# Kernel tuning notes

Measured on AMD Instinct MI355X. Metric: run time of the kernel, lower is better.

Reference implementation:

```python
import jax, jax.numpy as jnp
import numpy as np

N_NODES = 50000
N_EDGES = 1600000
IN_DIM = 256
HID = 128
HEADS = 1
N_CLASSES = 40
NEG_SLOPE = 0.2


def gat_conv(x, W, a_src, a_dst, b, src, dst, concat):
    """PyG GATConv (eval mode). x: [N, F_in]; W: [H*C, F_in]; a_*: [H, C]; b: bias."""
    N = x.shape[0]
    H, C = a_src.shape
    h = (x @ W.T).reshape(N, H, C)                       # [N, H, C]
    alpha_src = jnp.sum(h * a_src, axis=-1)              # [N, H]
    alpha_dst = jnp.sum(h * a_dst, axis=-1)              # [N, H]
    e = jax.nn.leaky_relu(alpha_src[src] + alpha_dst[dst], NEG_SLOPE)  # [E, H]
    # scatter-softmax over incoming edges of each destination node
    m = jax.ops.segment_max(e, dst, num_segments=N)
    m = jnp.where(jnp.isfinite(m), m, 0.0)               # nodes with no in-edges
    ex = jnp.exp(e - m[dst])
    denom = jax.ops.segment_sum(ex, dst, num_segments=N)
    alpha = ex / jnp.maximum(denom[dst], 1e-16)          # [E, H]
    out = jax.ops.segment_sum(h[src] * alpha[..., None], dst, num_segments=N)  # [N, H, C]
    out = out.reshape(N, H * C) if concat else out.mean(axis=1)
    return out + b


def setup_inputs() -> dict:
    key = jax.random.key(0)
    ks = jax.random.split(key, 10)
    glorot = lambda k, shape: jax.random.normal(k, shape, jnp.float32) * np.sqrt(2.0 / (shape[0] + shape[-1]))
    x = jax.random.normal(ks[0], (N_NODES, IN_DIM), jnp.float32)
    edge_index = jax.random.randint(ks[1], (2, N_EDGES), 0, N_NODES, jnp.int64)
    # layer 0: in=IN_DIM -> hidden, heads=HEADS, concat=True
    W0 = glorot(ks[2], (HEADS * HID, IN_DIM))
    a_src0 = glorot(ks[3], (HEADS, HID))
    a_dst0 = glorot(ks[4], (HEADS, HID))
    b0 = jnp.zeros((HEADS * HID,), jnp.float32)
    # layer 1: in=hidden*heads -> n_classes, concat=False
    W1 = glorot(ks[5], (HEADS * N_CLASSES, HEADS * HID))
    a_src1 = glorot(ks[6], (HEADS, N_CLASSES))
    a_dst1 = glorot(ks[7], (HEADS, N_CLASSES))
    b1 = jnp.zeros((N_CLASSES,), jnp.float32)
    return {"x": x, "edge_index": edge_index,
            "W0": W0, "a_src0": a_src0, "a_dst0": a_dst0, "b0": b0,
            "W1": W1, "a_src1": a_src1, "a_dst1": a_dst1, "b1": b1}


def reference(x, edge_index, W0, a_src0, a_dst0, b0, W1, a_src1, a_dst1, b1):
    N = x.shape[0]
    # PyG GATConv default add_self_loops=True (each layer adds them transiently)
    loop = jnp.arange(N, dtype=edge_index.dtype)
    src = jnp.concatenate([edge_index[0], loop])
    dst = jnp.concatenate([edge_index[1], loop])
    h = gat_conv(x, W0, a_src0, a_dst0, b0, src, dst, concat=True)
    h = jax.nn.relu(h)  # dropout is identity in eval mode
    out = gat_conv(h, W1, a_src1, a_dst1, b1, src, dst, concat=False)
    return out
```

## Files before the change

### kernel.cpp

```cpp
#include <hip/hip_runtime.h>
#include <hip/hip_bf16.h>

#define N_NODES 50000
#define N_EDGES 1600000
#define ET (N_EDGES + N_NODES)
#define IN_DIM 256
#define HID 128
#define NCLS 40
#define NEG 0.2f
#define NBUCK 391
#define CHUNK 4096
#define CAP 5120
#define SCATB ((ET + CHUNK - 1) / CHUNK)
#define GEMMB ((N_NODES + 63) / 64)

typedef short bf16x8 __attribute__((ext_vector_type(8)));
typedef float f32x4  __attribute__((ext_vector_type(4)));

__device__ __forceinline__ unsigned pk2(float a, float b) {
    __hip_bfloat16 ha = __float2bfloat16(a), hb = __float2bfloat16(b);
    unsigned short ua = *(unsigned short*)&ha, ub = *(unsigned short*)&hb;
    return (unsigned)ua | ((unsigned)ub << 16);
}
__device__ __forceinline__ float blo(unsigned u) { return __uint_as_float(u << 16); }
__device__ __forceinline__ float bhi(unsigned u) { return __uint_as_float(u & 0xffff0000u); }

__global__ void k_init(int* __restrict__ cursor) {
    int i = blockIdx.x * 256 + threadIdx.x;
    if (i < NBUCK) cursor[i] = i * CAP;
}

__global__ __launch_bounds__(256) void k_fused(
    const int* __restrict__ ei, int* __restrict__ cursor, unsigned int* __restrict__ buf,
    const float* __restrict__ x, const float* __restrict__ W0,
    const float* __restrict__ a_s, const float* __restrict__ a_d,
    unsigned short* __restrict__ h0b, float* __restrict__ as0, float* __restrict__ ad0) {
    __shared__ unsigned pool[6912];
    int t = threadIdx.x;

    if (blockIdx.x < SCATB) {
        int* sd    = (int*)pool;
        int* hist  = (int*)pool + 4096;
        int* wbase = (int*)pool + 4487;
        for (int i = t; i < NBUCK; i += 256) hist[i] = 0;
        __syncthreads();
        int base = blockIdx.x * CHUNK;
        #pragma unroll
        for (int j = 0; j < 16; ++j) {
            int i = base + j * 256 + t;
            int d = -1;
            if (i < ET) d = (i < N_EDGES) ? ei[N_EDGES + i] : (i - N_EDGES);
            sd[j * 256 + t] = d;
            if (d >= 0) atomicAdd(&hist[d >> 7], 1);
        }
        __syncthreads();
        for (int i = t; i < NBUCK; i += 256) {
            int h = hist[i];
            wbase[i] = h ? atomicAdd(&cursor[i], h) : 0;
            hist[i] = 0;
        }
        __syncthreads();
        #pragma unroll
        for (int j = 0; j < 16; ++j) {
            int i = base + j * 256 + t;
            int d = sd[j * 256 + t];
            if (d >= 0) {
                int s_ = (i < N_EDGES) ? ei[i] : d;
                int b = d >> 7;
                int off = atomicAdd(&hist[b], 1);
                buf[wbase[b] + off] = ((unsigned)(d & 127) << 16) | (unsigned)s_;
            }
        }
        return;
    }

    unsigned* sA = pool;
    unsigned* sB = pool + 2304;
    int n0 = (blockIdx.x - SCATB) * 64;
    int w = t >> 6, lane = t & 63;
    int rw = lane & 15, q = lane >> 4;
    f32x4 acc[8];
    #pragma unroll
    for (int n = 0; n < 8; ++n) acc[n] = (f32x4){0.f, 0.f, 0.f, 0.f};

    for (int kc = 0; kc < IN_DIM; kc += 64) {
        #pragma unroll
        for (int i = 0; i < 4; ++i) {
            int f = i * 256 + t;
            int r = f >> 4, fq = f & 15;
            float4 v = make_float4(0.f, 0.f, 0.f, 0.f);
            if (n0 + r < N_NODES)
                v = *(const float4*)&x[(size_t)(n0 + r) * IN_DIM + kc + fq * 4];
            *(uint2*)&sA[r * 36 + fq * 2] = make_uint2(pk2(v.x, v.y), pk2(v.z, v.w));
        }
        #pragma unroll
        for (int i = 0; i < 8; ++i) {
            int f = i * 256 + t;
            int c = f >> 4, fq = f & 15;
            float4 v = *(const float4*)&W0[(size_t)c * IN_DIM + kc + fq * 4];
            *(uint2*)&sB[c * 36 + fq * 2] = make_uint2(pk2(v.x, v.y), pk2(v.z, v.w));
        }
        __syncthreads();
        #pragma unroll
        for (int ks = 0; ks < 2; ++ks) {
            bf16x8 af = *(const bf16x8*)((const unsigned short*)sA + (16 * w + rw) * 72 + ks * 32 + q * 8);
            #pragma unroll
            for (int n = 0; n < 8; ++n) {
                bf16x8 bfr = *(const bf16x8*)((const unsigned short*)sB + (n * 16 + rw) * 72 + ks * 32 + q * 8);
                acc[n] = __builtin_amdgcn_mfma_f32_16x16x32_bf16(af, bfr, acc[n], 0, 0, 0);
            }
        }
        __syncthreads();
    }

    float asv[8], adv[8];
    #pragma unroll
    for (int n = 0; n < 8; ++n) { asv[n] = a_s[n * 16 + rw]; adv[n] = a_d[n * 16 + rw]; }
    float ps[4] = {0.f, 0.f, 0.f, 0.f}, pd[4] = {0.f, 0.f, 0.f, 0.f};
    #pragma unroll
    for (int n = 0; n < 8; ++n)
        #pragma unroll
        for (int reg = 0; reg < 4; ++reg) {
            float vv = acc[n][reg];
            ps[reg] += vv * asv[n];
            pd[reg] += vv * adv[n];
        }
    #pragma unroll
    for (int reg = 0; reg < 4; ++reg) {
        int node = n0 + 16 * w + q * 4 + reg;
        if (node < N_NODES) {
            #pragma unroll
            for (int n = 0; n < 8; ++n) {
                __hip_bfloat16 hb = __float2bfloat16(acc[n][reg]);
                h0b[(size_t)node * HID + n * 16 + rw] = *(unsigned short*)&hb;
            }
        }
    }
    #pragma unroll
    for (int reg = 0; reg < 4; ++reg)
        #pragma unroll
        for (int off = 1; off < 16; off <<= 1) {
            ps[reg] += __shfl_xor(ps[reg], off);
            pd[reg] += __shfl_xor(pd[reg], off);
        }
    if (rw == 0) {
        #pragma unroll
        for (int reg = 0; reg < 4; ++reg) {
            int node = n0 + 16 * w + q * 4 + reg;
            if (node < N_NODES) { as0[node] = ps[reg]; ad0[node] = pd[reg]; }
        }
    }
}

__global__ __launch_bounds__(256) void k_bucket_build(const unsigned int* __restrict__ buf,
                                                      const int* __restrict__ cursor,
                                                      int* __restrict__ rp, int* __restrict__ re,
                                                      int* __restrict__ csr) {
    __shared__ int cnt[128], rpl[128], cur[128];
    int b = blockIdx.x;
    int t = threadIdx.x;
    int lo = b * CAP, hi = cursor[b];
    if (t < 128) cnt[t] = 0;
    __syncthreads();
    for (int i = lo + t; i < hi; i += 256) atomicAdd(&cnt[buf[i] >> 16], 1);
    __syncthreads();
    if (t == 0) {
        int run = 0;
        #pragma unroll
        for (int l = 0; l < 128; ++l) { rpl[l] = run; run += cnt[l]; }
    }
    __syncthreads();
    if (t < 128) {
        int node = b * 128 + t;
        if (node < N_NODES) { rp[node] = lo + rpl[t]; re[node] = lo + rpl[t] + cnt[t]; }
        cur[t] = 0;
    }
    __syncthreads();
    for (int i = lo + t; i < hi; i += 256) {
        unsigned v = buf[i];
        int dl = v >> 16;
        int off = atomicAdd(&cur[dl], 1);
        csr[lo + rpl[dl] + off] = (int)(v & 0xffffu);
    }
}

__global__ __launch_bounds__(256) void k_agg0(
    const uint4* __restrict__ h0q, const float* __restrict__ as, const float* __restrict__ ad,
    const int* __restrict__ rp, const int* __restrict__ re, const int* __restrict__ csr,
    const float* __restrict__ bias, unsigned short* __restrict__ actb) {
    __shared__ float sw_[4][64];
    __shared__ int   ss_[4][64];
    int wid = threadIdx.x >> 6, lane = threadIdx.x & 63;
    int q = lane >> 4, ql = lane & 15;
    int node = blockIdx.x * 4 + wid;
    int start = rp[node], end = re[node];
    float ad_n = ad[node];
    float a0 = 0.f, a1 = 0.f, a2 = 0.f, a3 = 0.f;
    float a4 = 0.f, a5 = 0.f, a6 = 0.f, a7 = 0.f, den = 0.f;
    for (int base = start; base < end; base += 64) {
        int mm = end - base; if (mm > 64) mm = 64;
        int s_l = 0; float w_l = 0.f;
        if (lane < mm) {
            s_l = csr[base + lane];
            float e = as[s_l] + ad_n;
            e = (e > 0.f) ? e : NEG * e;
            w_l = __expf(e);
            den += w_l;
        }
        ss_[wid][lane] = s_l;
        sw_[wid][lane] = w_l;
        for (int jj = 0; jj < mm; jj += 16) {
            int i0 = jj + q, i1 = i0 + 4, i2 = i0 + 8, i3 = i0 + 12;
            int   s0 = ss_[wid][i0], s1 = ss_[wid][i1], s2 = ss_[wid][i2], s3 = ss_[wid][i3];
            float w0 = sw_[wid][i0], w1 = sw_[wid][i1], w2 = sw_[wid][i2], w3 = sw_[wid][i3];
            uint4 u0 = h0q[(size_t)s0 * 16 + ql];
            uint4 u1 = h0q[(size_t)s1 * 16 + ql];
            uint4 u2 = h0q[(size_t)s2 * 16 + ql];
            uint4 u3 = h0q[(size_t)s3 * 16 + ql];
            a0 += w0 * blo(u0.x) + w1 * blo(u1.x) + w2 * blo(u2.x) + w3 * blo(u3.x);
            a1 += w0 * bhi(u0.x) + w1 * bhi(u1.x) + w2 * bhi(u2.x) + w3 * bhi(u3.x);
            a2 += w0 * blo(u0.y) + w1 * blo(u1.y) + w2 * blo(u2.y) + w3 * blo(u3.y);
            a3 += w0 * bhi(u0.y) + w1 * bhi(u1.y) + w2 * bhi(u2.y) + w3 * bhi(u3.y);
            a4 += w0 * blo(u0.z) + w1 * blo(u1.z) + w2 * blo(u2.z) + w3 * blo(u3.z);
            a5 += w0 * bhi(u0.z) + w1 * bhi(u1.z) + w2 * bhi(u2.z) + w3 * bhi(u3.z);
            a6 += w0 * blo(u0.w) + w1 * blo(u1.w) + w2 * blo(u2.w) + w3 * blo(u3.w);
            a7 += w0 * bhi(u0.w) + w1 * bhi(u1.w) + w2 * bhi(u2.w) + w3 * bhi(u3.w);
        }
    }
    #pragma unroll
    for (int off = 32; off; off >>= 1) den += __shfl_xor(den, off);
    a0 += __shfl_xor(a0, 16); a0 += __shfl_xor(a0, 32);
    a1 += __shfl_xor(a1, 16); a1 += __shfl_xor(a1, 32);
    a2 += __shfl_xor(a2, 16); a2 += __shfl_xor(a2, 32);
    a3 += __shfl_xor(a3, 16); a3 += __shfl_xor(a3, 32);
    a4 += __shfl_xor(a4, 16); a4 += __shfl_xor(a4, 32);
    a5 += __shfl_xor(a5, 16); a5 += __shfl_xor(a5, 32);
    a6 += __shfl_xor(a6, 16); a6 += __shfl_xor(a6, 32);
    a7 += __shfl_xor(a7, 16); a7 += __shfl_xor(a7, 32);
    if (lane < 16) {
        float inv = 1.f / fmaxf(den, 1e-16f);
        float4 b0v = *(const float4*)&bias[ql * 8];
        float4 b1v = *(const float4*)&bias[ql * 8 + 4];
        float r0 = fmaxf(a0 * inv + b0v.x, 0.f);
        float r1 = fmaxf(a1 * inv + b0v.y, 0.f);
        float r2 = fmaxf(a2 * inv + b0v.z, 0.f);
        float r3 = fmaxf(a3 * inv + b0v.w, 0.f);
        float r4 = fmaxf(a4 * inv + b1v.x, 0.f);
        float r5 = fmaxf(a5 * inv + b1v.y, 0.f);
        float r6 = fmaxf(a6 * inv + b1v.z, 0.f);
        float r7 = fmaxf(a7 * inv + b1v.w, 0.f);
        *(uint4*)&actb[(size_t)node * HID + ql * 8] =
            make_uint4(pk2(r0, r1), pk2(r2, r3), pk2(r4, r5), pk2(r6, r7));
    }
}

__global__ __launch_bounds__(128) void k_gemm1(
    const unsigned short* __restrict__ actb, const float* __restrict__ W1,
    const float* __restrict__ a_s, const float* __restrict__ a_d,
    unsigned short* __restrict__ h1b, float* __restrict__ as1, float* __restrict__ ad1) {
    __shared__ float w1l[NCLS * HID];
    __shared__ float av[NCLS], adv[NCLS];
    int t = threadIdx.x;
    #pragma unroll
    for (int i = 0; i < 10; ++i) {
        int j = t + 128 * i;
        ((float4*)w1l)[j] = ((const float4*)W1)[j];
    }
    if (t < NCLS) { av[t] = a_s[t]; adv[t] = a_d[t]; }
    __syncthreads();
    int n = blockIdx.x * 128 + t;
    if (n >= N_NODES) return;
    const uint4* ar = (const uint4*)(actb + (size_t)n * HID);
    float acc[NCLS];
    #pragma unroll
    for (int c = 0; c < NCLS; ++c) acc[c] = 0.f;
    for (int k0 = 0; k0 < HID; k0 += 8) {
        uint4 v = ar[k0 >> 3];
        float x0 = blo(v.x), x1 = bhi(v.x), x2 = blo(v.y), x3 = bhi(v.y);
        float x4 = blo(v.z), x5 = bhi(v.z), x6 = blo(v.w), x7 = bhi(v.w);
        #pragma unroll
        for (int c = 0; c < NCLS; ++c) {
            const float* wr = &w1l[c * HID + k0];
            acc[c] += x0 * wr[0] + x1 * wr[1] + x2 * wr[2] + x3 * wr[3]
                    + x4 * wr[4] + x5 * wr[5] + x6 * wr[6] + x7 * wr[7];
        }
    }
    float ps = 0.f, pd = 0.f;
    #pragma unroll
    for (int c = 0; c < NCLS; ++c) { ps += acc[c] * av[c]; pd += acc[c] * adv[c]; }
    unsigned pk_[20];
    #pragma unroll
    for (int c = 0; c < 20; ++c) pk_[c] = pk2(acc[2 * c], acc[2 * c + 1]);
    #pragma unroll
    for (int i = 0; i < 5; ++i)
        *(uint4*)&h1b[(size_t)n * NCLS + i * 8] = make_uint4(pk_[4*i], pk_[4*i+1], pk_[4*i+2], pk_[4*i+3]);
    as1[n] = ps; ad1[n] = pd;
}

__global__ __launch_bounds__(256) void k_agg1(
    const uint2* __restrict__ h1u, const float* __restrict__ as, const float* __restrict__ ad,
    const int* __restrict__ rp, const int* __restrict__ re, const int* __restrict__ csr,
    const float* __restrict__ bias, float* __restrict__ out) {
    __shared__ float sw_[4][64];
    __shared__ int   ss_[4][64];
    int wid = threadIdx.x >> 6, lane = threadIdx.x & 63;
    int q = lane >> 4, ql = lane & 15;
    int off10 = (ql < 10) ? ql : 0;
    int node = blockIdx.x * 4 + wid;
    int start = rp[node], end = re[node];
    float ad_n = ad[node];
    float a0 = 0.f, a1 = 0.f, a2 = 0.f, a3 = 0.f, den = 0.f;
    for (int base = start; base < end; base += 64) {
        int mm = end - base; if (mm > 64) mm = 64;
        int s_l = 0; float w_l = 0.f;
        if (lane < mm) {
            s_l = csr[base + lane];
            float e = as[s_l] + ad_n;
            e = (e > 0.f) ? e : NEG * e;
            w_l = __expf(e);
            den += w_l;
        }
        ss_[wid][lane] = s_l;
        sw_[wid][lane] = w_l;
        for (int jj = 0; jj < mm; jj += 16) {
            int i0 = jj + q, i1 = i0 + 4, i2 = i0 + 8, i3 = i0 + 12;
            int   s0 = ss_[wid][i0], s1 = ss_[wid][i1], s2 = ss_[wid][i2], s3 = ss_[wid][i3];
            float w0 = sw_[wid][i0], w1 = sw_[wid][i1], w2 = sw_[wid][i2], w3 = sw_[wid][i3];
            uint2 u0 = h1u[(size_t)s0 * 10 + off10];
            uint2 u1 = h1u[(size_t)s1 * 10 + off10];
            uint2 u2 = h1u[(size_t)s2 * 10 + off10];
            uint2 u3 = h1u[(size_t)s3 * 10 + off10];
            a0 += w0 * blo(u0.x) + w1 * blo(u1.x) + w2 * blo(u2.x) + w3 * blo(u3.x);
            a1 += w0 * bhi(u0.x) + w1 * bhi(u1.x) + w2 * bhi(u2.x) + w3 * bhi(u3.x);
            a2 += w0 * blo(u0.y) + w1 * blo(u1.y) + w2 * blo(u2.y) + w3 * blo(u3.y);
            a3 += w0 * bhi(u0.y) + w1 * bhi(u1.y) + w2 * bhi(u2.y) + w3 * bhi(u3.y);
        }
    }
    #pragma unroll
    for (int off = 32; off; off >>= 1) den += __shfl_xor(den, off);
    a0 += __shfl_xor(a0, 16); a0 += __shfl_xor(a0, 32);
    a1 += __shfl_xor(a1, 16); a1 += __shfl_xor(a1, 32);
    a2 += __shfl_xor(a2, 16); a2 += __shfl_xor(a2, 32);
    a3 += __shfl_xor(a3, 16); a3 += __shfl_xor(a3, 32);
    if (lane < 10) {
        float inv = 1.f / fmaxf(den, 1e-16f);
        float4 b4 = *(const float4*)&bias[ql * 4];
        float4 r;
        r.x = a0 * inv + b4.x;
        r.y = a1 * inv + b4.y;
        r.z = a2 * inv + b4.z;
        r.w = a3 * inv + b4.w;
        *(float4*)&out[(size_t)node * NCLS + ql * 4] = r;
    }
}

extern "C" void kernel_launch(void* const* d_in, const int* in_sizes, int n_in,
                              void* d_out, int out_size, void* d_ws, size_t ws_size,
                              hipStream_t stream) {
    const float* x    = (const float*)d_in[0];
    const int*   ei   = (const int*)d_in[1];
    const float* W0   = (const float*)d_in[2];
    const float* a_s0 = (const float*)d_in[3];
    const float* a_d0 = (const float*)d_in[4];
    const float* b0   = (const float*)d_in[5];
    const float* W1   = (const float*)d_in[6];
    const float* a_s1 = (const float*)d_in[7];
    const float* a_d1 = (const float*)d_in[8];
    const float* b1   = (const float*)d_in[9];

    char* p = (char*)d_ws;
    auto alloc = [&](size_t bytes) { void* q = p; p += (bytes + 255) & ~size_t(255); return q; };
    unsigned short* h0b  = (unsigned short*)alloc((size_t)N_NODES * HID * 2);
    unsigned int*   buf  = (unsigned int*)alloc((size_t)NBUCK * CAP * 4);
    int*   csr    = (int*)alloc((size_t)NBUCK * CAP * 4);
    unsigned short* h1b  = (unsigned short*)alloc(((size_t)N_NODES * NCLS + 32) * 2);
    unsigned short* actb = (unsigned short*)alloc((size_t)N_NODES * HID * 2);
    float* as0    = (float*)alloc((size_t)N_NODES * 4);
    float* ad0    = (float*)alloc((size_t)N_NODES * 4);
    float* as1    = (float*)alloc((size_t)N_NODES * 4);
    float* ad1    = (float*)alloc((size_t)N_NODES * 4);
    int*   rp     = (int*)alloc((size_t)N_NODES * 4);
    int*   re     = (int*)alloc((size_t)N_NODES * 4);
    int*   cursor = (int*)alloc((size_t)NBUCK * 4);

    k_init<<<(NBUCK + 255) / 256, 256, 0, stream>>>(cursor);
    k_fused<<<SCATB + GEMMB, 256, 0, stream>>>(ei, cursor, buf, x, W0, a_s0, a_d0, h0b, as0, ad0);
    k_bucket_build<<<NBUCK, 256, 0, stream>>>(buf, cursor, rp, re, csr);
    k_agg0<<<N_NODES / 4, 256, 0, stream>>>((const uint4*)h0b, as0, ad0, rp, re, csr, b0, actb);
    k_gemm1<<<(N_NODES + 127) / 128, 128, 0, stream>>>(actb, W1, a_s1, a_d1, h1b, as1, ad1);
    k_agg1<<<N_NODES / 4, 256, 0, stream>>>((const uint2*)h1b, as1, ad1, rp, re, csr, b1, (float*)d_out);
}
```

Before: 271.3 us.

## Merge all stages into one persistent cooperative kernel with grid syncs

Replaces the six separate kernel launches with a single cooperative persistent kernel. The scatter/GEMM, CSR bucket build, layer-0 aggregation, layer-1 GEMM and layer-1 aggregation each run as a grid-stride phase, separated by grid.sync(). The grid is sized from the occupancy query, with launch bounds set to 4 blocks per CU. This is meant to remove launch overhead and inter-kernel gaps. In exchange it adds grid-wide barriers, lower per-phase occupancy, and register pressure from holding every phase in one kernel.

```diff
diff --git a/kernel.cpp b/kernel.cpp
--- a/kernel.cpp
+++ b/kernel.cpp
@@ -1,5 +1,8 @@
 #include <hip/hip_runtime.h>
 #include <hip/hip_bf16.h>
+#include <hip/hip_cooperative_groups.h>
+
+namespace cg = cooperative_groups;
 
 #define N_NODES 50000
 #define N_EDGES 1600000
@@ -25,332 +28,341 @@
 __device__ __forceinline__ float blo(unsigned u) { return __uint_as_float(u << 16); }
 __device__ __forceinline__ float bhi(unsigned u) { return __uint_as_float(u & 0xffff0000u); }
 
-__global__ void k_init(int* __restrict__ cursor) {
-    int i = blockIdx.x * 256 + threadIdx.x;
-    if (i < NBUCK) cursor[i] = i * CAP;
-}
-
-__global__ __launch_bounds__(256) void k_fused(
+__global__ __launch_bounds__(256, 4) void k_mega(
     const int* __restrict__ ei, int* __restrict__ cursor, unsigned int* __restrict__ buf,
     const float* __restrict__ x, const float* __restrict__ W0,
-    const float* __restrict__ a_s, const float* __restrict__ a_d,
-    unsigned short* __restrict__ h0b, float* __restrict__ as0, float* __restrict__ ad0) {
+    const float* __restrict__ a_s0, const float* __restrict__ a_d0,
+    unsigned short* __restrict__ h0b, float* __restrict__ as0, float* __restrict__ ad0,
+    int* __restrict__ rp, int* __restrict__ re, int* __restrict__ csr,
+    const float* __restrict__ b0, unsigned short* __restrict__ actb,
+    const float* __restrict__ W1, const float* __restrict__ a_s1, const float* __restrict__ a_d1,
+    unsigned short* __restrict__ h1b, float* __restrict__ as1, float* __restrict__ ad1,
+    const float* __restrict__ b1, float* __restrict__ out) {
     __shared__ unsigned pool[6912];
-    int t = threadIdx.x;
-
-    if (blockIdx.x < SCATB) {
-        int* sd    = (int*)pool;
-        int* hist  = (int*)pool + 4096;
-        int* wbase = (int*)pool + 4487;
-        for (int i = t; i < NBUCK; i += 256) hist[i] = 0;
-        __syncthreads();
-        int base = blockIdx.x * CHUNK;
+    cg::grid_group grid = cg::this_grid();
+    const int t = threadIdx.x;
+    const int nb = gridDim.x;
+
+    for (int task = blockIdx.x; task < SCATB + GEMMB; task += nb) {
+        if (task < SCATB) {
+            int* sd    = (int*)pool;
+            int* hist  = (int*)pool + 4096;
+            int* wbase = (int*)pool + 4487;
+            for (int i = t; i < NBUCK; i += 256) hist[i] = 0;
+            __syncthreads();
+            int base = task * CHUNK;
+            #pragma unroll
+            for (int j = 0; j < 16; ++j) {
+                int i = base + j * 256 + t;
+                int d = -1;
+                if (i < ET) d = (i < N_EDGES) ? ei[N_EDGES + i] : (i - N_EDGES);
+                sd[j * 256 + t] = d;
+                if (d >= 0) atomicAdd(&hist[d >> 7], 1);
+            }
+            __syncthreads();
+            for (int i = t; i < NBUCK; i += 256) {
+                int h = hist[i];
+                wbase[i] = i * CAP + (h ? atomicAdd(&cursor[i], h) : 0);
+                hist[i] = 0;
+            }
+            __syncthreads();
+            #pragma unroll
+            for (int j = 0; j < 16; ++j) {
+                int i = base + j * 256 + t;
+                int d = sd[j * 256 + t];
+                if (d >= 0) {
+                    int s_ = (i < N_EDGES) ? ei[i] : d;
+                    int bb = d >> 7;
+                    int off = atomicAdd(&hist[bb], 1);
+                    buf[wbase[bb] + off] = ((unsigned)(d & 127) << 16) | (unsigned)s_;
+                }
+            }
+        } else {
+            unsigned* sA = pool;
+            unsigned* sB = pool + 2304;
+            int n0 = (task - SCATB) * 64;
+            int w = t >> 6, lane = t & 63;
+            int rw = lane & 15, q = lane >> 4;
+            f32x4 acc[8];
+            #pragma unroll
+            for (int n = 0; n < 8; ++n) acc[n] = (f32x4){0.f, 0.f, 0.f, 0.f};
+            for (int kc = 0; kc < IN_DIM; kc += 64) {
+                #pragma unroll
+                for (int i = 0; i < 4; ++i) {
+                    int f = i * 256 + t;
+                    int r = f >> 4, fq = f & 15;
+                    float4 v = make_float4(0.f, 0.f, 0.f, 0.f);
+                    if (n0 + r < N_NODES)
+                        v = *(const float4*)&x[(size_t)(n0 + r) * IN_DIM + kc + fq * 4];
+                    *(uint2*)&sA[r * 36 + fq * 2] = make_uint2(pk2(v.x, v.y), pk2(v.z, v.w));
+                }
+                #pragma unroll
+                for (int i = 0; i < 8; ++i) {
+                    int f = i * 256 + t;
+                    int c = f >> 4, fq = f & 15;
+                    float4 v = *(const float4*)&W0[(size_t)c * IN_DIM + kc + fq * 4];
+                    *(uint2*)&sB[c * 36 + fq * 2] = make_uint2(pk2(v.x, v.y), pk2(v.z, v.w));
+                }
+                __syncthreads();
+                #pragma unroll
+                for (int ks = 0; ks < 2; ++ks) {
+                    bf16x8 af = *(const bf16x8*)((const unsigned short*)sA + (16 * w + rw) * 72 + ks * 32 + q * 8);
+                    #pragma unroll
+                    for (int n = 0; n < 8; ++n) {
+                        bf16x8 bfr = *(const bf16x8*)((const unsigned short*)sB + (n * 16 + rw) * 72 + ks * 32 + q * 8);
+                        acc[n] = __builtin_amdgcn_mfma_f32_16x16x32_bf16(af, bfr, acc[n], 0, 0, 0);
+                    }
+                }
+                __syncthreads();
+            }
+            float asv[8], adv[8];
+            #pragma unroll
+            for (int n = 0; n < 8; ++n) { asv[n] = a_s0[n * 16 + rw]; adv[n] = a_d0[n * 16 + rw]; }
+            float ps[4] = {0.f, 0.f, 0.f, 0.f}, pd[4] = {0.f, 0.f, 0.f, 0.f};
+            #pragma unroll
+            for (int n = 0; n < 8; ++n)
+                #pragma unroll
+                for (int reg = 0; reg < 4; ++reg) {
+                    float vv = acc[n][reg];
+                    ps[reg] += vv * asv[n];
+                    pd[reg] += vv * adv[n];
+                }
+            #pragma unroll
+            for (int reg = 0; reg < 4; ++reg) {
+                int node = n0 + 16 * w + q * 4 + reg;
+                if (node < N_NODES) {
+                    #pragma unroll
+                    for (int n = 0; n < 8; ++n) {
+                        __hip_bfloat16 hb = __float2bfloat16(acc[n][reg]);
+                        h0b[(size_t)node * HID + n * 16 + rw] = *(unsigned short*)&hb;
+                    }
+                }
+            }
+            #pragma unroll
+            for (int reg = 0; reg < 4; ++reg)
+                #pragma unroll
+                for (int off = 1; off < 16; off <<= 1) {
+                    ps[reg] += __shfl_xor(ps[reg], off);
+                    pd[reg] += __shfl_xor(pd[reg], off);
+                }
+            if (rw == 0) {
+                #pragma unroll
+                for (int reg = 0; reg < 4; ++reg) {
+                    int node = n0 + 16 * w + q * 4 + reg;
+                    if (node < N_NODES) { as0[node] = ps[reg]; ad0[node] = pd[reg]; }
+                }
+            }
+        }
+        __syncthreads();
+    }
+    grid.sync();
+
+    for (int b = blockIdx.x; b < NBUCK; b += nb) {
+        int* cnt = (int*)pool;
+        int* rpl = (int*)pool + 128;
+        int* cur = (int*)pool + 256;
+        int lo = b * CAP, hi = lo + cursor[b];
+        if (t < 128) cnt[t] = 0;
+        __syncthreads();
+        for (int i = lo + t; i < hi; i += 256) atomicAdd(&cnt[buf[i] >> 16], 1);
+        __syncthreads();
+        if (t == 0) {
+            int run = 0;
+            #pragma unroll
+            for (int l = 0; l < 128; ++l) { rpl[l] = run; run += cnt[l]; }
+        }
+        __syncthreads();
+        if (t < 128) {
+            int node = b * 128 + t;
+            if (node < N_NODES) { rp[node] = lo + rpl[t]; re[node] = lo + rpl[t] + cnt[t]; }
+            cur[t] = 0;
+        }
+        __syncthreads();
+        for (int i = lo + t; i < hi; i += 256) {
+            unsigned v = buf[i];
+            int dl = v >> 16;
+            int off = atomicAdd(&cur[dl], 1);
+            csr[lo + rpl[dl] + off] = (int)(v & 0xffffu);
+        }
+        __syncthreads();
+    }
+    grid.sync();
+
+    {
+        float* swp = (float*)pool;
+        int*   ssp = (int*)pool + 256;
+        const uint4* h0q = (const uint4*)h0b;
+        int wid = t >> 6, lane = t & 63;
+        int q = lane >> 4, ql = lane & 15;
+        for (int g = blockIdx.x; g < N_NODES / 4; g += nb) {
+            int node = g * 4 + wid;
+            int start = rp[node], end = re[node];
+            float ad_n = ad0[node];
+            float a0 = 0.f, a1 = 0.f, a2 = 0.f, a3 = 0.f;
+            float a4 = 0.f, a5 = 0.f, a6 = 0.f, a7 = 0.f, den = 0.f;
+            for (int base = start; base < end; base += 64) {
+                int mm = end - base; if (mm > 64) mm = 64;
+                int s_l = 0; float w_l = 0.f;
+                if (lane < mm) {
+                    s_l = csr[base + lane];
+                    float e = as0[s_l] + ad_n;
+                    e = (e > 0.f) ? e : NEG * e;
+                    w_l = __expf(e);
+                    den += w_l;
+                }
+                ssp[wid * 64 + lane] = s_l;
+                swp[wid * 64 + lane] = w_l;
+                for (int jj = 0; jj < mm; jj += 16) {
+                    int i0 = jj + q, i1 = i0 + 4, i2 = i0 + 8, i3 = i0 + 12;
+                    int   s0 = ssp[wid * 64 + i0], s1 = ssp[wid * 64 + i1];
+                    int   s2 = ssp[wid * 64 + i2], s3 = ssp[wid * 64 + i3];
+                    float w0 = swp[wid * 64 + i0], w1 = swp[wid * 64 + i1];
+                    float w2 = swp[wid * 64 + i2], w3 = swp[wid * 64 + i3];
+                    uint4 u0 = h0q[(size_t)s0 * 16 + ql];
+                    uint4 u1 = h0q[(size_t)s1 * 16 + ql];
+                    uint4 u2 = h0q[(size_t)s2 * 16 + ql];
+                    uint4 u3 = h0q[(size_t)s3 * 16 + ql];
+                    a0 += w0 * blo(u0.x) + w1 * blo(u1.x) + w2 * blo(u2.x) + w3 * blo(u3.x);
+                    a1 += w0 * bhi(u0.x) + w1 * bhi(u1.x) + w2 * bhi(u2.x) + w3 * bhi(u3.x);
+                    a2 += w0 * blo(u0.y) + w1 * blo(u1.y) + w2 * blo(u2.y) + w3 * blo(u3.y);
+                    a3 += w0 * bhi(u0.y) + w1 * bhi(u1.y) + w2 * bhi(u2.y) + w3 * bhi(u3.y);
+                    a4 += w0 * blo(u0.z) + w1 * blo(u1.z) + w2 * blo(u2.z) + w3 * blo(u3.z);
+                    a5 += w0 * bhi(u0.z) + w1 * bhi(u1.z) + w2 * bhi(u2.z) + w3 * bhi(u3.z);
+                    a6 += w0 * blo(u0.w) + w1 * blo(u1.w) + w2 * blo(u2.w) + w3 * blo(u3.w);
+                    a7 += w0 * bhi(u0.w) + w1 * bhi(u1.w) + w2 * bhi(u2.w) + w3 * bhi(u3.w);
+                }
+            }
+            #pragma unroll
+            for (int off = 32; off; off >>= 1) den += __shfl_xor(den, off);
+            a0 += __shfl_xor(a0, 16); a0 += __shfl_xor(a0, 32);
+            a1 += __shfl_xor(a1, 16); a1 += __shfl_xor(a1, 32);
+            a2 += __shfl_xor(a2, 16); a2 += __shfl_xor(a2, 32);
+            a3 += __shfl_xor(a3, 16); a3 += __shfl_xor(a3, 32);
+            a4 += __shfl_xor(a4, 16); a4 += __shfl_xor(a4, 32);
+            a5 += __shfl_xor(a5, 16); a5 += __shfl_xor(a5, 32);
+            a6 += __shfl_xor(a6, 16); a6 += __shfl_xor(a6, 32);
+            a7 += __shfl_xor(a7, 16); a7 += __shfl_xor(a7, 32);
+            if (lane < 16) {
+                float inv = 1.f / fmaxf(den, 1e-16f);
+                float4 b0v = *(const float4*)&b0[ql * 8];
+                float4 b1v = *(const float4*)&b0[ql * 8 + 4];
+                float r0 = fmaxf(a0 * inv + b0v.x, 0.f);
+                float r1 = fmaxf(a1 * inv + b0v.y, 0.f);
+                float r2 = fmaxf(a2 * inv + b0v.z, 0.f);
+                float r3 = fmaxf(a3 * inv + b0v.w, 0.f);
+                float r4 = fmaxf(a4 * inv + b1v.x, 0.f);
+                float r5 = fmaxf(a5 * inv + b1v.y, 0.f);
+                float r6 = fmaxf(a6 * inv + b1v.z, 0.f);
+                float r7 = fmaxf(a7 * inv + b1v.w, 0.f);
+                *(uint4*)&actb[(size_t)node * HID + ql * 8] =
+                    make_uint4(pk2(r0, r1), pk2(r2, r3), pk2(r4, r5), pk2(r6, r7));
+            }
+        }
+    }
+    grid.sync();
+
+    {
+        float* w1l = (float*)pool;
+        float* av  = (float*)pool + 5120;
+        float* adv = (float*)pool + 5160;
         #pragma unroll
-        for (int j = 0; j < 16; ++j) {
-            int i = base + j * 256 + t;
-            int d = -1;
-            if (i < ET) d = (i < N_EDGES) ? ei[N_EDGES + i] : (i - N_EDGES);
-            sd[j * 256 + t] = d;
-            if (d >= 0) atomicAdd(&hist[d >> 7], 1);
-        }
-        __syncthreads();
-        for (int i = t; i < NBUCK; i += 256) {
-            int h = hist[i];
-            wbase[i] = h ? atomicAdd(&cursor[i], h) : 0;
-            hist[i] = 0;
-        }
-        __syncthreads();
-        #pragma unroll
-        for (int j = 0; j < 16; ++j) {
-            int i = base + j * 256 + t;
-            int d = sd[j * 256 + t];
-            if (d >= 0) {
-                int s_ = (i < N_EDGES) ? ei[i] : d;
-                int b = d >> 7;
-                int off = atomicAdd(&hist[b], 1);
-                buf[wbase[b] + off] = ((unsigned)(d & 127) << 16) | (unsigned)s_;
-            }
-        }
-        return;
+        for (int i = 0; i < 5; ++i) {
+            int j = t + 256 * i;
+            ((float4*)w1l)[j] = ((const float4*)W1)[j];
+        }
+        if (t < NCLS) { av[t] = a_s1[t]; adv[t] = a_d1[t]; }
+        __syncthreads();
+        for (int g = blockIdx.x; g < (N_NODES + 255) / 256; g += nb) {
+            int n = g * 256 + t;
+            if (n < N_NODES) {
+                const uint4* ar = (const uint4*)(actb + (size_t)n * HID);
+                float acc[NCLS];
+                #pragma unroll
+                for (int c = 0; c < NCLS; ++c) acc[c] = 0.f;
+                for (int k0 = 0; k0 < HID; k0 += 8) {
+                    uint4 v = ar[k0 >> 3];
+                    float x0 = blo(v.x), x1 = bhi(v.x), x2 = blo(v.y), x3 = bhi(v.y);
+                    float x4 = blo(v.z), x5 = bhi(v.z), x6 = blo(v.w), x7 = bhi(v.w);
+                    #pragma unroll
+                    for (int c = 0; c < NCLS; ++c) {
+                        const float* wr = &w1l[c * HID + k0];
+                        acc[c] += x0 * wr[0] + x1 * wr[1] + x2 * wr[2] + x3 * wr[3]
+                                + x4 * wr[4] + x5 * wr[5] + x6 * wr[6] + x7 * wr[7];
+                    }
+                }
+                float ps = 0.f, pd = 0.f;
+                #pragma unroll
+                for (int c = 0; c < NCLS; ++c) { ps += acc[c] * av[c]; pd += acc[c] * adv[c]; }
+                unsigned pk_[20];
+                #pragma unroll
+                for (int c = 0; c < 20; ++c) pk_[c] = pk2(acc[2 * c], acc[2 * c + 1]);
+                #pragma unroll
+                for (int i = 0; i < 5; ++i)
+                    *(uint4*)&h1b[(size_t)n * NCLS + i * 8] =
+                        make_uint4(pk_[4*i], pk_[4*i+1], pk_[4*i+2], pk_[4*i+3]);
+                as1[n] = ps; ad1[n] = pd;
+            }
+        }
     }
-
-    unsigned* sA = pool;
-    unsigned* sB = pool + 2304;
-    int n0 = (blockIdx.x - SCATB) * 64;
-    int w = t >> 6, lane = t & 63;
-    int rw = lane & 15, q = lane >> 4;
-    f32x4 acc[8];
-    #pragma unroll
-    for (int n = 0; n < 8; ++n) acc[n] = (f32x4){0.f, 0.f, 0.f, 0.f};
-
-    for (int kc = 0; kc < IN_DIM; kc += 64) {
-        #pragma unroll
-        for (int i = 0; i < 4; ++i) {
-            int f = i * 256 + t;
-            int r = f >> 4, fq = f & 15;
-            float4 v = make_float4(0.f, 0.f, 0.f, 0.f);
-            if (n0 + r < N_NODES)
-                v = *(const float4*)&x[(size_t)(n0 + r) * IN_DIM + kc + fq * 4];
-            *(uint2*)&sA[r * 36 + fq * 2] = make_uint2(pk2(v.x, v.y), pk2(v.z, v.w));
-        }
-        #pragma unroll
-        for (int i = 0; i < 8; ++i) {
-            int f = i * 256 + t;
-            int c = f >> 4, fq = f & 15;
-            float4 v = *(const float4*)&W0[(size_t)c * IN_DIM + kc + fq * 4];
-            *(uint2*)&sB[c * 36 + fq * 2] = make_uint2(pk2(v.x, v.y), pk2(v.z, v.w));
-        }
-        __syncthreads();
-        #pragma unroll
-        for (int ks = 0; ks < 2; ++ks) {
-            bf16x8 af = *(const bf16x8*)((const unsigned short*)sA + (16 * w + rw) * 72 + ks * 32 + q * 8);
-            #pragma unroll
-            for (int n = 0; n < 8; ++n) {
-                bf16x8 bfr = *(const bf16x8*)((const unsigned short*)sB + (n * 16 + rw) * 72 + ks * 32 + q * 8);
-                acc[n] = __builtin_amdgcn_mfma_f32_16x16x32_bf16(af, bfr, acc[n], 0, 0, 0);
-            }
-        }
-        __syncthreads();
-    }
-
-    float asv[8], adv[8];
-    #pragma unroll
-    for (int n = 0; n < 8; ++n) { asv[n] = a_s[n * 16 + rw]; adv[n] = a_d[n * 16 + rw]; }
-    float ps[4] = {0.f, 0.f, 0.f, 0.f}, pd[4] = {0.f, 0.f, 0.f, 0.f};
-    #pragma unroll
-    for (int n = 0; n < 8; ++n)
-        #pragma unroll
-        for (int reg = 0; reg < 4; ++reg) {
-            float vv = acc[n][reg];
-            ps[reg] += vv * asv[n];
-            pd[reg] += vv * adv[n];
-        }
-    #pragma unroll
-    for (int reg = 0; reg < 4; ++reg) {
-        int node = n0 + 16 * w + q * 4 + reg;
-        if (node < N_NODES) {
-            #pragma unroll
-            for (int n = 0; n < 8; ++n) {
-                __hip_bfloat16 hb = __float2bfloat16(acc[n][reg]);
-                h0b[(size_t)node * HID + n * 16 + rw] = *(unsigned short*)&hb;
-            }
-        }
-    }
-    #pragma unroll
-    for (int reg = 0; reg < 4; ++reg)
-        #pragma unroll
-        for (int off = 1; off < 16; off <<= 1) {
-            ps[reg] += __shfl_xor(ps[reg], off);
-            pd[reg] += __shfl_xor(pd[reg], off);
-        }
-    if (rw == 0) {
-        #pragma unroll
-        for (int reg = 0; reg < 4; ++reg) {
-            int node = n0 + 16 * w + q * 4 + reg;
-            if (node < N_NODES) { as0[node] = ps[reg]; ad0[node] = pd[reg]; }
-        }
-    }
-}
-
-__global__ __launch_bounds__(256) void k_bucket_build(const unsigned int* __restrict__ buf,
-                                                      const int* __restrict__ cursor,
-                                                      int* __restrict__ rp, int* __restrict__ re,
-                                                      int* __restrict__ csr) {
-    __shared__ int cnt[128], rpl[128], cur[128];
-    int b = blockIdx.x;
-    int t = threadIdx.x;
-    int lo = b * CAP, hi = cursor[b];
-    if (t < 128) cnt[t] = 0;
-    __syncthreads();
-    for (int i = lo + t; i < hi; i += 256) atomicAdd(&cnt[buf[i] >> 16], 1);
-    __syncthreads();
-    if (t == 0) {
-        int run = 0;
-        #pragma unroll
-        for (int l = 0; l < 128; ++l) { rpl[l] = run; run += cnt[l]; }
-    }
-    __syncthreads();
-    if (t < 128) {
-        int node = b * 128 + t;
-        if (node < N_NODES) { rp[node] = lo + rpl[t]; re[node] = lo + rpl[t] + cnt[t]; }
-        cur[t] = 0;
-    }
-    __syncthreads();
-    for (int i = lo + t; i < hi; i += 256) {
-        unsigned v = buf[i];
-        int dl = v >> 16;
-        int off = atomicAdd(&cur[dl], 1);
-        csr[lo + rpl[dl] + off] = (int)(v & 0xffffu);
-    }
-}
-
-__global__ __launch_bounds__(256) void k_agg0(
-    const uint4* __restrict__ h0q, const float* __restrict__ as, const float* __restrict__ ad,
-    const int* __restrict__ rp, const int* __restrict__ re, const int* __restrict__ csr,
-    const float* __restrict__ bias, unsigned short* __restrict__ actb) {
-    __shared__ float sw_[4][64];
-    __shared__ int   ss_[4][64];
-    int wid = threadIdx.x >> 6, lane = threadIdx.x & 63;
-    int q = lane >> 4, ql = lane & 15;
-    int node = blockIdx.x * 4 + wid;
-    int start = rp[node], end = re[node];
-    float ad_n = ad[node];
-    float a0 = 0.f, a1 = 0.f, a2 = 0.f, a3 = 0.f;
-    float a4 = 0.f, a5 = 0.f, a6 = 0.f, a7 = 0.f, den = 0.f;
-    for (int base = start; base < end; base += 64) {
-        int mm = end - base; if (mm > 64) mm = 64;
-        int s_l = 0; float w_l = 0.f;
-        if (lane < mm) {
-            s_l = csr[base + lane];
-            float e = as[s_l] + ad_n;
-            e = (e > 0.f) ? e : NEG * e;
-            w_l = __expf(e);
-            den += w_l;
-        }
-        ss_[wid][lane] = s_l;
-        sw_[wid][lane] = w_l;
-        for (int jj = 0; jj < mm; jj += 16) {
-            int i0 = jj + q, i1 = i0 + 4, i2 = i0 + 8, i3 = i0 + 12;
-            int   s0 = ss_[wid][i0], s1 = ss_[wid][i1], s2 = ss_[wid][i2], s3 = ss_[wid][i3];
-            float w0 = sw_[wid][i0], w1 = sw_[wid][i1], w2 = sw_[wid][i2], w3 = sw_[wid][i3];
-            uint4 u0 = h0q[(size_t)s0 * 16 + ql];
-            uint4 u1 = h0q[(size_t)s1 * 16 + ql];
-            uint4 u2 = h0q[(size_t)s2 * 16 + ql];
-            uint4 u3 = h0q[(size_t)s3 * 16 + ql];
-            a0 += w0 * blo(u0.x) + w1 * blo(u1.x) + w2 * blo(u2.x) + w3 * blo(u3.x);
-            a1 += w0 * bhi(u0.x) + w1 * bhi(u1.x) + w2 * bhi(u2.x) + w3 * bhi(u3.x);
-            a2 += w0 * blo(u0.y) + w1 * blo(u1.y) + w2 * blo(u2.y) + w3 * blo(u3.y);
-            a3 += w0 * bhi(u0.y) + w1 * bhi(u1.y) + w2 * bhi(u2.y) + w3 * bhi(u3.y);
-            a4 += w0 * blo(u0.z) + w1 * blo(u1.z) + w2 * blo(u2.z) + w3 * blo(u3.z);
-            a5 += w0 * bhi(u0.z) + w1 * bhi(u1.z) + w2 * bhi(u2.z) + w3 * bhi(u3.z);
-            a6 += w0 * blo(u0.w) + w1 * blo(u1.w) + w2 * blo(u2.w) + w3 * blo(u3.w);
-            a7 += w0 * bhi(u0.w) + w1 * bhi(u1.w) + w2 * bhi(u2.w) + w3 * bhi(u3.w);
-        }
-    }
-    #pragma unroll
-    for (int off = 32; off; off >>= 1) den += __shfl_xor(den, off);
-    a0 += __shfl_xor(a0, 16); a0 += __shfl_xor(a0, 32);
-    a1 += __shfl_xor(a1, 16); a1 += __shfl_xor(a1, 32);
-    a2 += __shfl_xor(a2, 16); a2 += __shfl_xor(a2, 32);
-    a3 += __shfl_xor(a3, 16); a3 += __shfl_xor(a3, 32);
-    a4 += __shfl_xor(a4, 16); a4 += __shfl_xor(a4, 32);
-    a5 += __shfl_xor(a5, 16); a5 += __shfl_xor(a5, 32);
-    a6 += __shfl_xor(a6, 16); a6 += __shfl_xor(a6, 32);
-    a7 += __shfl_xor(a7, 16); a7 += __shfl_xor(a7, 32);
-    if (lane < 16) {
-        float inv = 1.f / fmaxf(den, 1e-16f);
-        float4 b0v = *(const float4*)&bias[ql * 8];
-        float4 b1v = *(const float4*)&bias[ql * 8 + 4];
-        float r0 = fmaxf(a0 * inv + b0v.x, 0.f);
-        float r1 = fmaxf(a1 * inv + b0v.y, 0.f);
-        float r2 = fmaxf(a2 * inv + b0v.z, 0.f);
-        float r3 = fmaxf(a3 * inv + b0v.w, 0.f);
-        float r4 = fmaxf(a4 * inv + b1v.x, 0.f);
-        float r5 = fmaxf(a5 * inv + b1v.y, 0.f);
-        float r6 = fmaxf(a6 * inv + b1v.z, 0.f);
-        float r7 = fmaxf(a7 * inv + b1v.w, 0.f);
-        *(uint4*)&actb[(size_t)node * HID + ql * 8] =
-            make_uint4(pk2(r0, r1), pk2(r2, r3), pk2(r4, r5), pk2(r6, r7));
-    }
-}
-
-__global__ __launch_bounds__(128) void k_gemm1(
-    const unsigned short* __restrict__ actb, const float* __restrict__ W1,
-    const float* __restrict__ a_s, const float* __restrict__ a_d,
-    unsigned short* __restrict__ h1b, float* __restrict__ as1, float* __restrict__ ad1) {
-    __shared__ float w1l[NCLS * HID];
-    __shared__ float av[NCLS], adv[NCLS];
-    int t = threadIdx.x;
-    #pragma unroll
-    for (int i = 0; i < 10; ++i) {
-        int j = t + 128 * i;
-        ((float4*)w1l)[j] = ((const float4*)W1)[j];
-    }
-    if (t < NCLS) { av[t] = a_s[t]; adv[t] = a_d[t]; }
-    __syncthreads();
-    int n = blockIdx.x * 128 + t;
-    if (n >= N_NODES) return;
-    const uint4* ar = (const uint4*)(actb + (size_t)n * HID);
-    float acc[NCLS];
-    #pragma unroll
-    for (int c = 0; c < NCLS; ++c) acc[c] = 0.f;
-    for (int k0 = 0; k0 < HID; k0 += 8) {
-        uint4 v = ar[k0 >> 3];
-        float x0 = blo(v.x), x1 = bhi(v.x), x2 = blo(v.y), x3 = bhi(v.y);
-        float x4 = blo(v.z), x5 = bhi(v.z), x6 = blo(v.w), x7 = bhi(v.w);
-        #pragma unroll
-        for (int c = 0; c < NCLS; ++c) {
-            const float* wr = &w1l[c * HID + k0];
-            acc[c] += x0 * wr[0] + x1 * wr[1] + x2 * wr[2] + x3 * wr[3]
-                    + x4 * wr[4] + x5 * wr[5] + x6 * wr[6] + x7 * wr[7];
-        }
-    }
-    float ps = 0.f, pd = 0.f;
-    #pragma unroll
-    for (int c = 0; c < NCLS; ++c) { ps += acc[c] * av[c]; pd += acc[c] * adv[c]; }
-    unsigned pk_[20];
-    #pragma unroll
-    for (int c = 0; c < 20; ++c) pk_[c] = pk2(acc[2 * c], acc[2 * c + 1]);
-    #pragma unroll
-    for (int i = 0; i < 5; ++i)
-        *(uint4*)&h1b[(size_t)n * NCLS + i * 8] = make_uint4(pk_[4*i], pk_[4*i+1], pk_[4*i+2], pk_[4*i+3]);
-    as1[n] = ps; ad1[n] = pd;
-}
-
-__global__ __launch_bounds__(256) void k_agg1(
-    const uint2* __restrict__ h1u, const float* __restrict__ as, const float* __restrict__ ad,
-    const int* __restrict__ rp, const int* __restrict__ re, const int* __restrict__ csr,
-    const float* __restrict__ bias, float* __restrict__ out) {
-    __shared__ float sw_[4][64];
-    __shared__ int   ss_[4][64];
-    int wid = threadIdx.x >> 6, lane = threadIdx.x & 63;
-    int q = lane >> 4, ql = lane & 15;
-    int off10 = (ql < 10) ? ql : 0;
-    int node = blockIdx.x * 4 + wid;
-    int start = rp[node], end = re[node];
-    float ad_n = ad[node];
-    float a0 = 0.f, a1 = 0.f, a2 = 0.f, a3 = 0.f, den = 0.f;
-    for (int base = start; base < end; base += 64) {
-        int mm = end - base; if (mm > 64) mm = 64;
-        int s_l = 0; float w_l = 0.f;
-        if (lane < mm) {
-            s_l = csr[base + lane];
-            float e = as[s_l] + ad_n;
-            e = (e > 0.f) ? e : NEG * e;
-            w_l = __expf(e);
-            den += w_l;
-        }
-        ss_[wid][lane] = s_l;
-        sw_[wid][lane] = w_l;
-        for (int jj = 0; jj < mm; jj += 16) {
-            int i0 = jj + q, i1 = i0 + 4, i2 = i0 + 8, i3 = i0 + 12;
-            int   s0 = ss_[wid][i0], s1 = ss_[wid][i1], s2 = ss_[wid][i2], s3 = ss_[wid][i3];
-            float w0 = sw_[wid][i0], w1 = sw_[wid][i1], w2 = sw_[wid][i2], w3 = sw_[wid][i3];
-            uint2 u0 = h1u[(size_t)s0 * 10 + off10];
-            uint2 u1 = h1u[(size_t)s1 * 10 + off10];
-            uint2 u2 = h1u[(size_t)s2 * 10 + off10];
-            uint2 u3 = h1u[(size_t)s3 * 10 + off10];
-            a0 += w0 * blo(u0.x) + w1 * blo(u1.x) + w2 * blo(u2.x) + w3 * blo(u3.x);
-            a1 += w0 * bhi(u0.x) + w1 * bhi(u1.x) + w2 * bhi(u2.x) + w3 * bhi(u3.x);
-            a2 += w0 * blo(u0.y) + w1 * blo(u1.y) + w2 * blo(u2.y) + w3 * blo(u3.y);
-            a3 += w0 * bhi(u0.y) + w1 * bhi(u1.y) + w2 * bhi(u2.y) + w3 * bhi(u3.y);
-        }
-    }
-    #pragma unroll
-    for (int off = 32; off; off >>= 1) den += __shfl_xor(den, off);
-    a0 += __shfl_xor(a0, 16); a0 += __shfl_xor(a0, 32);
-    a1 += __shfl_xor(a1, 16); a1 += __shfl_xor(a1, 32);
-    a2 += __shfl_xor(a2, 16); a2 += __shfl_xor(a2, 32);
-    a3 += __shfl_xor(a3, 16); a3 += __shfl_xor(a3, 32);
-    if (lane < 10) {
-        float inv = 1.f / fmaxf(den, 1e-16f);
-        float4 b4 = *(const float4*)&bias[ql * 4];
-        float4 r;
-        r.x = a0 * inv + b4.x;
-        r.y = a1 * inv + b4.y;
-        r.z = a2 * inv + b4.z;
-        r.w = a3 * inv + b4.w;
-        *(float4*)&out[(size_t)node * NCLS + ql * 4] = r;
+    grid.sync();
+
+    {
+        float* swp = (float*)pool;
+        int*   ssp = (int*)pool + 256;
+        const uint2* h1u = (const uint2*)h1b;
+        int wid = t >> 6, lane = t & 63;
+        int q = lane >> 4, ql = lane & 15;
+        int off10 = (ql < 10) ? ql : 0;
+        for (int g = blockIdx.x; g < N_NODES / 4; g += nb) {
+            int node = g * 4 + wid;
+            int start = rp[node], end = re[node];
+            float ad_n = ad1[node];
+            float a0 = 0.f, a1 = 0.f, a2 = 0.f, a3 = 0.f, den = 0.f;
+            for (int base = start; base < end; base += 64) {
+                int mm = end - base; if (mm > 64) mm = 64;
+                int s_l = 0; float w_l = 0.f;
+                if (lane < mm) {
+                    s_l = csr[base + lane];
+                    float e = as1[s_l] + ad_n;
+                    e = (e > 0.f) ? e : NEG * e;
+                    w_l = __expf(e);
+                    den += w_l;
+                }
+                ssp[wid * 64 + lane] = s_l;
+                swp[wid * 64 + lane] = w_l;
+                for (int jj = 0; jj < mm; jj += 16) {
+                    int i0 = jj + q, i1 = i0 + 4, i2 = i0 + 8, i3 = i0 + 12;
+                    int   s0 = ssp[wid * 64 + i0], s1 = ssp[wid * 64 + i1];
+                    int   s2 = ssp[wid * 64 + i2], s3 = ssp[wid * 64 + i3];
+                    float w0 = swp[wid * 64 + i0], w1 = swp[wid * 64 + i1];
+                    float w2 = swp[wid * 64 + i2], w3 = swp[wid * 64 + i3];
+                    uint2 u0 = h1u[(size_t)s0 * 10 + off10];
+                    uint2 u1 = h1u[(size_t)s1 * 10 + off10];
+                    uint2 u2 = h1u[(size_t)s2 * 10 + off10];
+                    uint2 u3 = h1u[(size_t)s3 * 10 + off10];
+                    a0 += w0 * blo(u0.x) + w1 * blo(u1.x) + w2 * blo(u2.x) + w3 * blo(u3.x);
+                    a1 += w0 * bhi(u0.x) + w1 * bhi(u1.x) + w2 * bhi(u2.x) + w3 * bhi(u3.x);
+                    a2 += w0 * blo(u0.y) + w1 * blo(u1.y) + w2 * blo(u2.y) + w3 * blo(u3.y);
+                    a3 += w0 * bhi(u0.y) + w1 * bhi(u1.y) + w2 * bhi(u2.y) + w3 * bhi(u3.y);
+                }
+            }
+            #pragma unroll
+            for (int off = 32; off; off >>= 1) den += __shfl_xor(den, off);
+            a0 += __shfl_xor(a0, 16); a0 += __shfl_xor(a0, 32);
+            a1 += __shfl_xor(a1, 16); a1 += __shfl_xor(a1, 32);
+            a2 += __shfl_xor(a2, 16); a2 += __shfl_xor(a2, 32);
+            a3 += __shfl_xor(a3, 16); a3 += __shfl_xor(a3, 32);
+            if (lane < 10) {
+                float inv = 1.f / fmaxf(den, 1e-16f);
+                float4 b4 = *(const float4*)&b1[ql * 4];
+                float4 r;
+                r.x = a0 * inv + b4.x;
+                r.y = a1 * inv + b4.y;
+                r.z = a2 * inv + b4.z;
+                r.w = a3 * inv + b4.w;
+                *(float4*)&out[(size_t)node * NCLS + ql * 4] = r;
+            }
+        }
     }
 }
 
@@ -382,11 +394,24 @@
     int*   rp     = (int*)alloc((size_t)N_NODES * 4);
     int*   re     = (int*)alloc((size_t)N_NODES * 4);
     int*   cursor = (int*)alloc((size_t)NBUCK * 4);
-
-    k_init<<<(NBUCK + 255) / 256, 256, 0, stream>>>(cursor);
-    k_fused<<<SCATB + GEMMB, 256, 0, stream>>>(ei, cursor, buf, x, W0, a_s0, a_d0, h0b, as0, ad0);
-    k_bucket_build<<<NBUCK, 256, 0, stream>>>(buf, cursor, rp, re, csr);
-    k_agg0<<<N_NODES / 4, 256, 0, stream>>>((const uint4*)h0b, as0, ad0, rp, re, csr, b0, actb);
-    k_gemm1<<<(N_NODES + 127) / 128, 128, 0, stream>>>(actb, W1, a_s1, a_d1, h1b, as1, ad1);
-    k_agg1<<<N_NODES / 4, 256, 0, stream>>>((const uint2*)h1b, as1, ad1, rp, re, csr, b1, (float*)d_out);
+    float* outp   = (float*)d_out;
+
+    hipMemsetAsync(cursor, 0, (size_t)NBUCK * 4, stream);
+
+    int mpc = 0;
+    hipOccupancyMaxActiveBlocksPerMultiprocessor(&mpc, (const void*)k_mega, 256, 0);
+    if (mpc < 1) mpc = 1;
+    long long grid = (long long)mpc * 256;
+    if (grid > 2048) grid = 2048;
+
+    void* args[] = { (void*)&ei, (void*)&cursor, (void*)&buf,
+                     (void*)&x, (void*)&W0, (void*)&a_s0, (void*)&a_d0,
+                     (void*)&h0b, (void*)&as0, (void*)&ad0,
+                     (void*)&rp, (void*)&re, (void*)&csr,
+                     (void*)&b0, (void*)&actb,
+                     (void*)&W1, (void*)&a_s1, (void*)&a_d1,
+                     (void*)&h1b, (void*)&as1, (void*)&ad1,
+                     (void*)&b1, (void*)&outp };
+    hipLaunchCooperativeKernel((const void*)k_mega, dim3((unsigned)grid), dim3(256),
+                               args, 0, stream);
 }
```

After: 801.2 us. 195% more time.
